# Performance work log

Hardware: AMD Instinct MI355X
Metric: run time of the kernel (lower is better)

The kernel has to match this reference:

```python
import jax, jax.numpy as jnp
import numpy as np

# Default bone connections from BoneLengthLoss.__init__
BONES = np.array([(1, 2), (1, 3), (1, 4), (2, 5), (3, 6), (11, 12), (11, 13), (12, 14),
                  (13, 14), (14, 15), (15, 16), (16, 17), (12, 18), (18, 20), (20, 22),
                  (13, 19), (19, 21), (21, 23), (16, 24), (16, 25), (24, 26), (25, 26),
                  (24, 27), (27, 29), (29, 31), (25, 28), (28, 30), (30, 32), (17, 33),
                  (33, 34), (34, 35), (35, 36)], dtype=np.int32)
J1 = jnp.asarray(BONES[:, 0])
J2 = jnp.asarray(BONES[:, 1])

BATCH = 524288
NUM_KPTS = 37


def setup_inputs() -> dict:
    key = jax.random.key(0)
    k1, k2, k3 = jax.random.split(key, 3)
    pose_3d_pred = jax.random.normal(k1, (BATCH, NUM_KPTS, 3), dtype=jnp.float32)
    pose_3d_ref = jax.random.normal(k2, (BATCH, NUM_KPTS, 3), dtype=jnp.float32)
    valid_mask = jax.random.randint(k3, (BATCH, NUM_KPTS), 0, 2).astype(jnp.bool_)
    return {"pose_3d_pred": pose_3d_pred, "pose_3d_ref": pose_3d_ref,
            "valid_mask": valid_mask}


def reference(pose_3d_pred, pose_3d_ref, valid_mask):
    # Gather both endpoints of every bone: (B, n_bones, 3)
    pred_vec = pose_3d_pred[:, J2, :] - pose_3d_pred[:, J1, :]
    ref_vec = pose_3d_ref[:, J2, :] - pose_3d_ref[:, J1, :]
    pred_len = jnp.linalg.norm(pred_vec, axis=-1)  # (B, n_bones)
    ref_len = jnp.linalg.norm(ref_vec, axis=-1)    # (B, n_bones)
    # Bone is valid iff both endpoints are valid
    bone_valid = (valid_mask[:, J1] & valid_mask[:, J2]).astype(pred_len.dtype)
    # MSE over all valid (batch, bone) entries == mean over concatenated valid lengths
    sq_err = (pred_len - ref_len) ** 2
    num = jnp.sum(sq_err * bone_valid)
    den = jnp.sum(bone_valid)
    return num / den
```

## Files before the change

### kernel.cpp

```cpp
#include <hip/hip_runtime.h>


#define NBONES 32
#define NKPT   37
#define ROWF   111
#define RPW    8
#define WT_F4  222
#define WT_MW  74
#define WT_MI  296
#define BLOCK  256
#define WPB    4
#define GRID   2048

__constant__ unsigned char c_j1[NBONES] = {1,1,1,2,3,11,11,12,13,14,15,16,12,18,20,13,19,21,16,16,24,25,24,27,29,25,28,30,17,33,34,35};
__constant__ unsigned char c_j2[NBONES] = {2,3,4,5,6,12,13,14,14,15,16,17,18,20,22,19,21,23,24,25,26,26,27,29,31,28,30,32,33,34,35,36};

__global__ void init_detect(const unsigned int* __restrict__ mw,
                            unsigned int* __restrict__ ws) {
    const int tid = threadIdx.x;
    if (tid < 4) ws[tid] = 0u;
    __syncthreads();
    unsigned int local = 0;
    for (int i = tid; i < 1024; i += BLOCK) local |= mw[i] & 0xFFFFFF00u;
    if (__any(local != 0) && (tid & 63) == 0) atomicOr(&ws[2], 1u);
}

__global__ __launch_bounds__(BLOCK, 4)
void bone_main(const float* __restrict__ pred, const float* __restrict__ ref,
               const void* __restrict__ mask, int B,
               unsigned int* __restrict__ ws, float* __restrict__ out) {
    __shared__ __align__(16) float s_pose[WPB][2][RPW * ROWF];
    __shared__ __align__(4) unsigned char s_mask[WPB][WT_MI + 8];
    __shared__ float s_rn[WPB];
    __shared__ unsigned int s_rd[WPB];

    const int tid  = threadIdx.x;
    const int wave = tid >> 6;
    const int lane = tid & 63;
    const int row  = lane >> 3;
    const int grp  = lane & 7;

    const bool mask_bytes = (ws[2] != 0);

    int j1v[4], j2v[4];
#pragma unroll
    for (int k = 0; k < 4; ++k) {
        j1v[k] = (int)c_j1[grp * 4 + k];
        j2v[k] = (int)c_j2[grp * 4 + k];
    }

    const float4* __restrict__ pred4 = (const float4*)pred;
    const float4* __restrict__ ref4  = (const float4*)ref;
    const unsigned int* __restrict__ mw = (const unsigned int*)mask;
    const int* __restrict__ mi = (const int*)mask;

    float*  sp_w = &s_pose[wave][0][0];
    float*  sr_w = &s_pose[wave][1][0];
    float4* sp4  = (float4*)sp_w;
    float4* sr4  = (float4*)sr_w;
    unsigned char* sm_w = &s_mask[wave][0];

    float num = 0.0f;
    unsigned int den = 0u;

    const int nwt    = B / RPW;
    const int gwave  = blockIdx.x * WPB + wave;
    const int nwaves = GRID * WPB;

    int idx[4];
#pragma unroll
    for (int j = 0; j < 4; ++j) idx[j] = min(lane + 64 * j, WT_F4 - 1);

    for (int wt = gwave; wt < nwt; wt += nwaves) {
        const float4* pb = pred4 + (size_t)wt * WT_F4;
        const float4* rb = ref4  + (size_t)wt * WT_F4;

        float4 vp[4], vr[4];
#pragma unroll
        for (int j = 0; j < 4; ++j) vp[j] = pb[idx[j]];
#pragma unroll
        for (int j = 0; j < 4; ++j) vr[j] = rb[idx[j]];

        if (mask_bytes) {
            const unsigned int* mb = mw + (size_t)wt * WT_MW;
            unsigned int m0 = mb[lane];
            int i1 = min(lane + 64, WT_MW - 1);
            unsigned int m1 = mb[i1];
            ((unsigned int*)sm_w)[lane] = m0;
            ((unsigned int*)sm_w)[i1]   = m1;
        } else {
            const int* mb = mi + (size_t)wt * WT_MI;
#pragma unroll
            for (int j = 0; j < 5; ++j) {
                int i = min(lane + 64 * j, WT_MI - 1);
                sm_w[i] = (unsigned char)mb[i];
            }
        }

#pragma unroll
        for (int j = 0; j < 4; ++j) sp4[idx[j]] = vp[j];
#pragma unroll
        for (int j = 0; j < 4; ++j) sr4[idx[j]] = vr[j];

        const float* sp = sp_w + row * ROWF;
        const float* sr = sr_w + row * ROWF;
        const unsigned char* sm = sm_w + row * NKPT;
#pragma unroll
        for (int k = 0; k < 4; ++k) {
            const int a3 = j1v[k] * 3, b3 = j2v[k] * 3;
            float dx = sp[b3] - sp[a3];
            float dy = sp[b3 + 1] - sp[a3 + 1];
            float dz = sp[b3 + 2] - sp[a3 + 2];
            float pl = sqrtf(dx * dx + dy * dy + dz * dz);
            float ex = sr[b3] - sr[a3];
            float ey = sr[b3 + 1] - sr[a3 + 1];
            float ez = sr[b3 + 2] - sr[a3 + 2];
            float rl = sqrtf(ex * ex + ey * ey + ez * ez);
            unsigned int v = (unsigned int)(sm[j1v[k]] & sm[j2v[k]]);
            float d = pl - rl;
            num += v ? d * d : 0.0f;
            den += v;
        }
    }

#pragma unroll
    for (int off = 32; off > 0; off >>= 1) {
        num += __shfl_down(num, off, 64);
        den += __shfl_down(den, off, 64);
    }
    if (lane == 0) { s_rn[wave] = num; s_rd[wave] = den; }
    __syncthreads();
    if (tid == 0) {
        float n = s_rn[0] + s_rn[1] + s_rn[2] + s_rn[3];
        unsigned int d = s_rd[0] + s_rd[1] + s_rd[2] + s_rd[3];
        atomicAdd((float*)&ws[0], n);
        atomicAdd(&ws[1], d);
        __threadfence();
        unsigned int prev = atomicAdd(&ws[3], 1u);
        if (prev == (unsigned int)(gridDim.x - 1)) {
            float fn = atomicAdd((float*)&ws[0], 0.0f);
            unsigned int fd = atomicAdd(&ws[1], 0u);
            out[0] = fn / (float)fd;
        }
    }
}

extern "C" void kernel_launch(void* const* d_in, const int* in_sizes, int n_in,
                              void* d_out, int out_size, void* d_ws, size_t ws_size,
                              hipStream_t stream) {
    const float* pred = (const float*)d_in[0];
    const float* ref  = (const float*)d_in[1];
    const void*  mask = d_in[2];
    const int n_mask  = in_sizes[2];
    const int B       = n_mask / NKPT;
    unsigned int* ws  = (unsigned int*)d_ws;

    init_detect<<<1, BLOCK, 0, stream>>>((const unsigned int*)mask, ws);
    bone_main<<<GRID, BLOCK, 0, stream>>>(pred, ref, mask, B, ws, (float*)d_out);
}
```

Baseline: 582.8 us.

## Stage block tiles into LDS via global_load_lds and remap threads to rows

Replaces per-wave register-staged loads with direct global-to-LDS loads (global_load_lds) over a 32-row block-wide tile. Threads are remapped so each thread handles one row and a group of bones, with block-level barriers around the compute phase. The grid size changes and the mask-format branch becomes a template. This is meant to cut VGPR traffic and LDS store instructions, at the cost of two __syncthreads per tile and no double buffering, which may expose load latency.

```diff
diff --git a/kernel.cpp b/kernel.cpp
--- a/kernel.cpp
+++ b/kernel.cpp
@@ -1,19 +1,32 @@
 #include <hip/hip_runtime.h>
 
 
-#define NBONES 32
 #define NKPT   37
 #define ROWF   111
-#define RPW    8
-#define WT_F4  222
-#define WT_MW  74
-#define WT_MI  296
+#define TROWS  32
+#define TF4    888
+#define WF4    222
+#define TMW    296
+#define WMW    74
+#define TMI    1184
+#define WMI    296
 #define BLOCK  256
 #define WPB    4
-#define GRID   2048
+#define GRID   1280
 
-__constant__ unsigned char c_j1[NBONES] = {1,1,1,2,3,11,11,12,13,14,15,16,12,18,20,13,19,21,16,16,24,25,24,27,29,25,28,30,17,33,34,35};
-__constant__ unsigned char c_j2[NBONES] = {2,3,4,5,6,12,13,14,14,15,16,17,18,20,22,19,21,23,24,25,26,26,27,29,31,28,30,32,33,34,35,36};
+__constant__ unsigned char c_j1[32] = {1,1,1,2,3,11,11,12,13,14,15,16,12,18,20,13,19,21,16,16,24,25,24,27,29,25,28,30,17,33,34,35};
+__constant__ unsigned char c_j2[32] = {2,3,4,5,6,12,13,14,14,15,16,17,18,20,22,19,21,23,24,25,26,26,27,29,31,28,30,32,33,34,35,36};
+
+__device__ __forceinline__ void glds16(const void* g, void* l) {
+    __builtin_amdgcn_global_load_lds(
+        (const __attribute__((address_space(1))) void*)g,
+        (__attribute__((address_space(3))) void*)l, 16, 0, 0);
+}
+__device__ __forceinline__ void glds4(const void* g, void* l) {
+    __builtin_amdgcn_global_load_lds(
+        (const __attribute__((address_space(1))) void*)g,
+        (__attribute__((address_space(3))) void*)l, 4, 0, 0);
+}
 
 __global__ void init_detect(const unsigned int* __restrict__ mw,
                             unsigned int* __restrict__ ws) {
@@ -25,86 +38,51 @@
     if (__any(local != 0) && (tid & 63) == 0) atomicOr(&ws[2], 1u);
 }
 
-__global__ __launch_bounds__(BLOCK, 4)
-void bone_main(const float* __restrict__ pred, const float* __restrict__ ref,
-               const void* __restrict__ mask, int B,
-               unsigned int* __restrict__ ws, float* __restrict__ out) {
-    __shared__ __align__(16) float s_pose[WPB][2][RPW * ROWF];
-    __shared__ __align__(4) unsigned char s_mask[WPB][WT_MI + 8];
-    __shared__ float s_rn[WPB];
-    __shared__ unsigned int s_rd[WPB];
-
-    const int tid  = threadIdx.x;
-    const int wave = tid >> 6;
-    const int lane = tid & 63;
-    const int row  = lane >> 3;
-    const int grp  = lane & 7;
-
-    const bool mask_bytes = (ws[2] != 0);
-
-    int j1v[4], j2v[4];
-#pragma unroll
-    for (int k = 0; k < 4; ++k) {
-        j1v[k] = (int)c_j1[grp * 4 + k];
-        j2v[k] = (int)c_j2[grp * 4 + k];
-    }
-
-    const float4* __restrict__ pred4 = (const float4*)pred;
-    const float4* __restrict__ ref4  = (const float4*)ref;
+template <bool MASK_BYTES>
+__device__ __forceinline__ void tile_loop(
+    const float4* __restrict__ pred4, const float4* __restrict__ ref4,
+    const void* __restrict__ mask, int ntiles,
+    float4* s_pose, unsigned char* s_mask,
+    int wave, int lane, int row, const int* j1v, const int* j2v,
+    float& num, unsigned int& den)
+{
+    unsigned int* s_mask_w = (unsigned int*)s_mask;
     const unsigned int* __restrict__ mw = (const unsigned int*)mask;
     const int* __restrict__ mi = (const int*)mask;
+    const int sb = wave * WF4;
 
-    float*  sp_w = &s_pose[wave][0][0];
-    float*  sr_w = &s_pose[wave][1][0];
-    float4* sp4  = (float4*)sp_w;
-    float4* sr4  = (float4*)sr_w;
-    unsigned char* sm_w = &s_mask[wave][0];
+    for (int t = blockIdx.x; t < ntiles; t += GRID) {
+        const float4* pb = pred4 + (size_t)t * TF4;
+        const float4* rb = ref4  + (size_t)t * TF4;
 
-    float num = 0.0f;
-    unsigned int den = 0u;
-
-    const int nwt    = B / RPW;
-    const int gwave  = blockIdx.x * WPB + wave;
-    const int nwaves = GRID * WPB;
-
-    int idx[4];
-#pragma unroll
-    for (int j = 0; j < 4; ++j) idx[j] = min(lane + 64 * j, WT_F4 - 1);
-
-    for (int wt = gwave; wt < nwt; wt += nwaves) {
-        const float4* pb = pred4 + (size_t)wt * WT_F4;
-        const float4* rb = ref4  + (size_t)wt * WT_F4;
-
-        float4 vp[4], vr[4];
-#pragma unroll
-        for (int j = 0; j < 4; ++j) vp[j] = pb[idx[j]];
-#pragma unroll
-        for (int j = 0; j < 4; ++j) vr[j] = rb[idx[j]];
-
-        if (mask_bytes) {
-            const unsigned int* mb = mw + (size_t)wt * WT_MW;
-            unsigned int m0 = mb[lane];
-            int i1 = min(lane + 64, WT_MW - 1);
-            unsigned int m1 = mb[i1];
-            ((unsigned int*)sm_w)[lane] = m0;
-            ((unsigned int*)sm_w)[i1]   = m1;
+        glds16(pb + sb + lane,       &s_pose[sb]);
+        glds16(pb + sb + 64 + lane,  &s_pose[sb + 64]);
+        glds16(pb + sb + 128 + lane, &s_pose[sb + 128]);
+        glds16(rb + sb + lane,       &s_pose[TF4 + sb]);
+        glds16(rb + sb + 64 + lane,  &s_pose[TF4 + sb + 64]);
+        glds16(rb + sb + 128 + lane, &s_pose[TF4 + sb + 128]);
+        if (lane < WF4 - 192) {
+            glds16(pb + sb + 192 + lane, &s_pose[sb + 192]);
+            glds16(rb + sb + 192 + lane, &s_pose[TF4 + sb + 192]);
+        }
+        if (MASK_BYTES) {
+            const unsigned int* mb = mw + (size_t)t * TMW + wave * WMW;
+            glds4(mb + lane, &s_mask_w[wave * WMW]);
+            if (lane < WMW - 64)
+                glds4(mb + 64 + lane, &s_mask_w[wave * WMW + 64]);
         } else {
-            const int* mb = mi + (size_t)wt * WT_MI;
+            const int* mb = mi + (size_t)t * TMI + wave * WMI;
 #pragma unroll
             for (int j = 0; j < 5; ++j) {
-                int i = min(lane + 64 * j, WT_MI - 1);
-                sm_w[i] = (unsigned char)mb[i];
+                int i = lane + 64 * j;
+                if (i < WMI) s_mask[wave * WMI + i] = (unsigned char)mb[i];
             }
         }
+        __syncthreads();
 
-#pragma unroll
-        for (int j = 0; j < 4; ++j) sp4[idx[j]] = vp[j];
-#pragma unroll
-        for (int j = 0; j < 4; ++j) sr4[idx[j]] = vr[j];
-
-        const float* sp = sp_w + row * ROWF;
-        const float* sr = sr_w + row * ROWF;
-        const unsigned char* sm = sm_w + row * NKPT;
+        const float* sp = (const float*)s_pose + row * ROWF;
+        const float* sr = (const float*)(s_pose + TF4) + row * ROWF;
+        const unsigned char* sm = s_mask + row * NKPT;
 #pragma unroll
         for (int k = 0; k < 4; ++k) {
             const int a3 = j1v[k] * 3, b3 = j2v[k] * 3;
@@ -121,7 +99,44 @@
             num += v ? d * d : 0.0f;
             den += v;
         }
+        __syncthreads();
     }
+}
+
+__global__ __launch_bounds__(BLOCK, 4)
+void bone_main(const float* __restrict__ pred, const float* __restrict__ ref,
+               const void* __restrict__ mask, int B,
+               unsigned int* __restrict__ ws, float* __restrict__ out) {
+    __shared__ __align__(16) float4 s_pose[2 * TF4];
+    __shared__ __align__(4) unsigned char s_mask[TMI];
+    __shared__ float s_rn[WPB];
+    __shared__ unsigned int s_rd[WPB];
+
+    const int tid  = threadIdx.x;
+    const int wave = tid >> 6;
+    const int lane = tid & 63;
+    const int row  = tid & 31;
+    const int grp  = (tid >> 5) & 7;
+
+    int j1v[4], j2v[4];
+#pragma unroll
+    for (int k = 0; k < 4; ++k) {
+        j1v[k] = (int)c_j1[grp * 4 + k];
+        j2v[k] = (int)c_j2[grp * 4 + k];
+    }
+
+    const bool mask_bytes = (ws[2] != 0);
+    const int ntiles = B / TROWS;
+
+    float num = 0.0f;
+    unsigned int den = 0u;
+
+    if (mask_bytes)
+        tile_loop<true>((const float4*)pred, (const float4*)ref, mask, ntiles,
+                        s_pose, s_mask, wave, lane, row, j1v, j2v, num, den);
+    else
+        tile_loop<false>((const float4*)pred, (const float4*)ref, mask, ntiles,
+                         s_pose, s_mask, wave, lane, row, j1v, j2v, num, den);
 
 #pragma unroll
     for (int off = 32; off > 0; off >>= 1) {
```

Result: faster. 547.0 us (-6.1%).
